# Kernel optimization log

Hardware: AMD Instinct MI355X
Metric: run time of the kernel (lower is better)

## Reference

```python
import jax, jax.numpy as jnp
from jax import lax
import numpy as np

# Architecture constants (must match init_kwargs)
K = 3            # kernel_size
F = 128          # num_filters
NL = 4           # num_layers per stage
NS = 2           # num_stages (Decoder uses TCN(num_stages=2))
DILS = [2 ** l for _ in range(NS) for l in range(NL)]  # [1,2,4,8,1,2,4,8]
NB = NS * NL     # 8 residual blocks
C_IN = 32 + 1    # dec_feat + last_y channel
D_ENC = 128
T = 32           # target_len = max_seq_len
B = 64


def _cconv(x, w, d):
    # causal dilated conv1d; x: [B, L, Cin], w: [K, Cin, Cout]
    k = w.shape[0]
    return lax.conv_general_dilated(
        x, w, window_strides=(1,), padding=[((k - 1) * d, 0)],
        rhs_dilation=(d,), dimension_numbers=('NWC', 'WIO', 'NWC'))


def setup_inputs() -> dict:
    key = jax.random.key(0)
    ks = jax.random.split(key, 20)

    def he(k, shape, fan_in):
        return jax.random.normal(k, shape, jnp.float32) * np.sqrt(2.0 / fan_in)

    inp = {
        'data_encoder': jax.random.normal(ks[0], (B, 128, D_ENC), jnp.float32),
        'data_decoder': jax.random.normal(ks[1], (B, T, C_IN - 1), jnp.float32),
        'last_y': jax.random.normal(ks[2], (B,), jnp.float32),
        # TCN block 0 (input projection block)
        'w_in': he(ks[3], (K, C_IN, F), K * C_IN),
        'b_in': jnp.zeros((F,), jnp.float32),
        'w_res': he(ks[4], (1, C_IN, F), C_IN),
        'b_res': jnp.zeros((F,), jnp.float32),
        # conv1 of blocks 1..NB-1, conv2 of all blocks
        'w1': he(ks[5], (NB - 1, K, F, F), K * F),
        'b1': jnp.zeros((NB - 1, F), jnp.float32),
        'w2': he(ks[6], (NB, K, F, F), K * F),
        'b2': jnp.zeros((NB, F), jnp.float32),
        # dense head: (F + D_ENC) -> 128 -> 64 -> 1
        'wd0': he(ks[7], (F + D_ENC, 128), F + D_ENC),
        'bd0': jnp.zeros((128,), jnp.float32),
        'wd1': he(ks[8], (128, 64), 128),
        'bd1': jnp.zeros((64,), jnp.float32),
        'wd2': he(ks[9], (64, 1), 64),
        'bd2': jnp.zeros((1,), jnp.float32),
    }
    return inp


def reference(data_encoder, data_decoder, last_y,
              w_in, b_in, w_res, b_res, w1, b1, w2, b2,
              wd0, bd0, wd1, bd1, wd2, bd2) -> jnp.ndarray:
    elu = jax.nn.elu

    def tcn(x):
        # 2 stages x 4 residual blocks of dilated causal convs; dropout off (inference)
        h = x
        for b in range(NB):
            d = DILS[b]
            if b == 0:
                c = elu(_cconv(h, w_in, d) + b_in)
                res = _cconv(h, w_res, 1) + b_res  # 1x1 channel-matching projection
            else:
                c = elu(_cconv(h, w1[b - 1], d) + b1[b - 1])
                res = h
            c = elu(_cconv(c, w2[b], d) + b2[b])
            h = elu(c + res)
        return h  # [B, L, F]

    enc_last = data_encoder[:, -1:, :]  # [B, 1, D_ENC]

    def head(t):
        L = t.shape[1]
        o = jnp.concatenate(
            [t, jnp.broadcast_to(enc_last, (t.shape[0], L, D_ENC))], axis=-1)
        o = elu(o @ wd0 + bd0)
        o = elu(o @ wd1 + bd1)
        return o @ wd2 + bd2  # [B, L, 1]

    target_len = data_decoder.shape[1]
    ly = last_y.reshape(-1, 1, 1)  # [B, 1, 1]
    cur = jnp.concatenate([data_decoder[:, :1, :], ly], axis=-1)  # [B, 1, C_IN]

    preds = []
    for i in range(target_len):  # O(T^2): reruns full TCN on growing prefix
        out = head(tcn(cur))                 # [B, i+1, 1]
        preds.append(out[:, -1, :])          # [B, 1]
        if i < target_len - 1:
            last_preds = jnp.concatenate([ly, out], axis=1)  # [B, i+2, 1]
            cur = jnp.concatenate(
                [data_decoder[:, :i + 2, :], last_preds], axis=-1)
    return jnp.concatenate(preds, axis=1)  # [B, T]
```

## Files before the change

### kernel.cpp

```cpp
#include <hip/hip_runtime.h>
#include <hip/hip_fp16.h>


constexpr int OFF_WIN  = 0;
constexpr int OFF_WRES = 24576;
constexpr int OFF_W1   = 32768;
constexpr int OFF_W2   = 376832;
constexpr int OFF_WD0  = 770048;
constexpr int OFF_WD1  = 802816;
constexpr int OFF_WD2  = 811008;
constexpr int WS_HALFS = 811072;

constexpr int O_CURX = 0;
constexpr int O_ENC  = 64;
constexpr int O_H0   = 192;
constexpr int O_H1   = 320;
constexpr int O_C1A  = 448;
constexpr int O_C1B  = 576;
constexpr int O_RES  = 704;
constexpr int O_O1   = 832;
constexpr int O_O2   = 960;
constexpr int O_IN0  = 1024;
constexpr int O_IN1  = 1152;
constexpr int O_MID0 = 8576;
constexpr int SM_FLOATS = 16256;

__device__ __forceinline__ float elu1(float x) { return x > 0.f ? x : expm1f(x); }

__device__ __forceinline__ void bar() {
    __builtin_amdgcn_sched_barrier(0);
    asm volatile("s_waitcnt lgkmcnt(0)" ::: "memory");
    __builtin_amdgcn_s_barrier();
    __builtin_amdgcn_sched_barrier(0);
}

struct W4 { float4 v[4]; };
struct W2 { float4 v[2]; };

__device__ __forceinline__ void load4(W4& w, const __half* p) {
#pragma unroll
    for (int j = 0; j < 4; ++j) w.v[j] = *(const float4*)(p + j * 1024);
}
__device__ __forceinline__ void load2(W2& w, const __half* p, int stride) {
#pragma unroll
    for (int j = 0; j < 2; ++j) w.v[j] = *(const float4*)(p + j * stride);
}

__device__ __forceinline__ float dot8(float4 wv, const float* x) {
    const __half2* h = (const __half2*)&wv;
    float2 a = __half22float2(h[0]);
    float2 b = __half22float2(h[1]);
    float2 c = __half22float2(h[2]);
    float2 d = __half22float2(h[3]);
    float4 x0 = *(const float4*)(x);
    float4 x1 = *(const float4*)(x + 4);
    return a.x * x0.x + a.y * x0.y + b.x * x0.z + b.y * x0.w +
           c.x * x1.x + c.y * x1.y + d.x * x1.z + d.y * x1.w;
}
__device__ __forceinline__ float dot4j(const W4& w, const float* x, int ks) {
    float a = dot8(w.v[0], x + ks * 8);
    a += dot8(w.v[1], x + 32 + ks * 8);
    a += dot8(w.v[2], x + 64 + ks * 8);
    a += dot8(w.v[3], x + 96 + ks * 8);
    return a;
}
__device__ __forceinline__ float dot2j(const W2& w, const float* x, int ks) {
    return dot8(w.v[0], x + ks * 8) + dot8(w.v[1], x + 32 + ks * 8);
}

__device__ __forceinline__ void loadMain(W4& w0, W4& w1, W4& w2, const __half* base_lane, int ks) {
    load4(w0, base_lane + (ks * 4) * 1024);
    load4(w1, base_lane + ((4 + ks) * 4) * 1024);
    load4(w2, base_lane + ((8 + ks) * 4) * 1024);
}

template <bool FUSE>
__device__ __forceinline__ void computeMain(const W4& w0, const W4& w1, const W4& w2,
                                            const float* x2, const float* x1, const float* x0,
                                            const float* __restrict__ bias, float* dest,
                                            const float* resv, int ch, int ks, int lane) {
    float acc = dot4j(w0, x0, ks) + dot4j(w1, x1, ks) + dot4j(w2, x2, ks);
    acc += __shfl_xor(acc, 16, 64);
    acc += __shfl_xor(acc, 32, 64);
    float v = elu1(acc + bias[ch]);
    if (FUSE) v = elu1(v + resv[ch]);
    if (lane < 16) dest[ch] = v;
}

__global__ void prep_weights(const float* __restrict__ w_in, const float* __restrict__ w_res,
                             const float* __restrict__ w1, const float* __restrict__ w2,
                             const float* __restrict__ wd0, const float* __restrict__ wd1,
                             const float* __restrict__ wd2, __half* __restrict__ dst) {
    int i = blockIdx.x * blockDim.x + threadIdx.x;
    if (i >= WS_HALFS) return;
    float v = 0.f;
    if (i < OFF_WRES) {
        int q = i, e = q & 7, ch = (q >> 3) & 127, row = (q >> 10) & 7, k = q >> 13;
        int ks = row >> 1, j = row & 1, ci = j * 32 + ks * 8 + e;
        v = (ci < 33) ? w_in[(k * 33 + ci) * 128 + ch] : 0.f;
    } else if (i < OFF_W1) {
        int q = i - OFF_WRES, e = q & 7, ch = (q >> 3) & 127, row = (q >> 10) & 7;
        int ks = row >> 1, j = row & 1, ci = j * 32 + ks * 8 + e;
        v = (ci < 33) ? w_res[ci * 128 + ch] : 0.f;
    } else if (i < OFF_W2) {
        int r = i - OFF_W1, bb = r / 49152, q = r % 49152;
        int e = q & 7, ch = (q >> 3) & 127, row = (q >> 10) & 15, k = q >> 14;
        int ks = row >> 2, j = row & 3, ci = j * 32 + ks * 8 + e;
        v = w1[((size_t)(bb * 3 + k) * 128 + ci) * 128 + ch];
    } else if (i < OFF_WD0) {
        int r = i - OFF_W2, bb = r / 49152, q = r % 49152;
        int e = q & 7, ch = (q >> 3) & 127, row = (q >> 10) & 15, k = q >> 14;
        int ks = row >> 2, j = row & 3, ci = j * 32 + ks * 8 + e;
        v = w2[((size_t)(bb * 3 + k) * 128 + ci) * 128 + ch];
    } else if (i < OFF_WD1) {
        int q = i - OFF_WD0, e = q & 7, ch = (q >> 3) & 127, row = (q >> 10) & 31;
        int ks = row >> 3, j = row & 7, ci = j * 32 + ks * 8 + e;
        v = wd0[ci * 128 + ch];
    } else if (i < OFF_WD2) {
        int q = i - OFF_WD1, e = q & 7, ch = (q >> 3) & 63, row = (q >> 9) & 15;
        int ks8 = row >> 1, j = row & 1, ci = j * 64 + ks8 * 8 + e;
        v = wd1[ci * 64 + ch];
    } else {
        v = wd2[i - OFF_WD2];
    }
    dst[i] = __float2half(v);
}

__global__ __launch_bounds__(512) void decoder_stream(
    const float* __restrict__ enc, const float* __restrict__ dec,
    const float* __restrict__ last_y, const __half* __restrict__ wsh,
    const float* __restrict__ b_in, const float* __restrict__ b_res,
    const float* __restrict__ b1, const float* __restrict__ b2,
    const float* __restrict__ bd0, const float* __restrict__ bd1,
    const float* __restrict__ bd2, float* __restrict__ out) {
    __shared__ float sm[SM_FLOATS];
    const int tid = threadIdx.x;
    const int b = blockIdx.x;
    const int lane = tid & 63;
    const int wv = tid >> 6;
    const int ch = wv * 16 + (lane & 15);
    const int ks = lane >> 4;
    const int ch64 = wv * 8 + (lane & 7);
    const int ks8 = lane >> 3;

    for (int i = tid; i < SM_FLOATS; i += 512) sm[i] = 0.f;
    __syncthreads();
    if (tid < 128) sm[O_ENC + tid] = enc[((size_t)b * 128 + 127) * 128 + tid];
    if (tid < 32) sm[O_CURX + tid] = dec[((size_t)b * 32 + 0) * 32 + tid];
    if (tid == 32) sm[O_CURX + 32] = last_y[b];
    __syncthreads();

    const float bd2v = bd2[0];
    const float wd2r = (tid < 64) ? __half2float(wsh[OFF_WD2 + tid]) : 0.f;

    W4 A0, A1, A2, B0, B1, B2;
    W2 ia0, ia1, ia2, ir, D1w;

    {
        const __half* wl = wsh + OFF_WIN + ch * 8;
        load2(ia0, wl + (ks * 2) * 1024, 1024);
        load2(ia1, wl + (8 + ks * 2) * 1024, 1024);
        load2(ia2, wl + (16 + ks * 2) * 1024, 1024);
        load2(ir, wsh + OFF_WRES + ch * 8 + (ks * 2) * 1024, 1024);
    }

#pragma unroll 1
    for (int t = 0; t < 32; ++t) {
        {
            loadMain(B0, B1, B2, wsh + OFF_W2 + ch * 8, ks);
            const float* x1 = &sm[O_IN0 + ((t - 1) & 1) * 64];
            const float* x0 = &sm[O_IN0 + (t & 1) * 64];
            float aC = dot2j(ia0, x0, ks) + dot2j(ia1, x1, ks) + dot2j(ia2, &sm[O_CURX], ks);
            float aR = dot2j(ir, &sm[O_CURX], ks);
            aC += __shfl_xor(aC, 16, 64); aC += __shfl_xor(aC, 32, 64);
            aR += __shfl_xor(aR, 16, 64); aR += __shfl_xor(aR, 32, 64);
            if (lane < 16) {
                sm[O_C1A + ch] = elu1(aC + b_in[ch]);
                sm[O_RES + ch] = aR + b_res[ch];
            }
            bar();
        }
        {
            loadMain(A0, A1, A2, wsh + OFF_W1 + ch * 8, ks);
            if (tid < 64) sm[O_IN0 + (t & 1) * 64 + tid] = sm[O_CURX + tid];
            const float* m1 = &sm[O_MID0 + ((t - 1) & 1) * 128];
            const float* m0 = &sm[O_MID0 + (t & 1) * 128];
            computeMain<true>(B0, B1, B2, &sm[O_C1A], m1, m0, b2, &sm[O_H1], &sm[O_RES],
                              ch, ks, lane);
            bar();
        }
        int inB = O_IN1, midBprev = O_MID0, midB = O_MID0 + 256, mprev = 2;
#pragma unroll 1
        for (int blk = 1; blk < 8; ++blk) {
            const int d = 1 << (blk & 3);
            const int m = 2 * d;
            const int p = blk & 1;
            float* Hp = &sm[p ? O_H1 : O_H0];
            float* Hq = &sm[p ? O_H0 : O_H1];
            float* C1p = &sm[p ? O_C1B : O_C1A];
            float* C1q = &sm[p ? O_C1A : O_C1B];
            loadMain(B0, B1, B2, wsh + OFF_W2 + blk * 49152 + ch * 8, ks);
            if (tid < 128) sm[midBprev + (t & (mprev - 1)) * 128 + tid] = C1q[tid];
            {
                const float* x1 = &sm[inB + ((t - d) & (m - 1)) * 128];
                const float* x0 = &sm[inB + (t & (m - 1)) * 128];
                computeMain<false>(A0, A1, A2, Hp, x1, x0, b1 + (blk - 1) * 128, C1p, Hp,
                                   ch, ks, lane);
            }
            bar();
            if (blk < 7) {
                loadMain(A0, A1, A2, wsh + OFF_W1 + blk * 49152 + ch * 8, ks);
            } else {
                const __half* pd0 = wsh + OFF_WD0 + ch * 8;
                load4(A0, pd0 + (ks * 8) * 1024);
                load4(A1, pd0 + (ks * 8 + 4) * 1024);
            }
            if (tid < 128) sm[inB + (t & (m - 1)) * 128 + tid] = Hp[tid];
            {
                const float* m1 = &sm[midB + ((t - d) & (m - 1)) * 128];
                const float* m0 = &sm[midB + (t & (m - 1)) * 128];
                computeMain<true>(B0, B1, B2, C1p, m1, m0, b2 + blk * 128, Hq, Hp,
                                  ch, ks, lane);
            }
            bar();
            inB += m * 128; midBprev = midB; midB += m * 128; mprev = m;
        }
        {
            const __half* pd1 = wsh + OFF_WD1 + ch64 * 8 + (ks8 * 2) * 512;
            load2(D1w, pd1, 512);
            if (tid < 128) sm[midBprev + (t & (mprev - 1)) * 128 + tid] = sm[O_C1B + tid];
            float acc = dot4j(A0, &sm[O_H0], ks) + dot4j(A1, &sm[O_ENC], ks);
            acc += __shfl_xor(acc, 16, 64);
            acc += __shfl_xor(acc, 32, 64);
            if (lane < 16) sm[O_O1 + ch] = elu1(acc + bd0[ch]);
            bar();
        }
        {
            const __half* wl = wsh + OFF_WIN + ch * 8;
            load2(ia0, wl + (ks * 2) * 1024, 1024);
            load2(ia1, wl + (8 + ks * 2) * 1024, 1024);
            load2(ia2, wl + (16 + ks * 2) * 1024, 1024);
            load2(ir, wsh + OFF_WRES + ch * 8 + (ks * 2) * 1024, 1024);
            float acc = dot8(D1w.v[0], &sm[O_O1 + ks8 * 8]) +
                        dot8(D1w.v[1], &sm[O_O1 + 64 + ks8 * 8]);
            acc += __shfl_xor(acc, 8, 64);
            acc += __shfl_xor(acc, 16, 64);
            acc += __shfl_xor(acc, 32, 64);
            if (lane < 8) sm[O_O2 + ch64] = elu1(acc + bd1[ch64]);
            int tn = t < 31 ? t + 1 : 31;
            if (tid < 32) sm[O_CURX + tid] = dec[((size_t)b * 32 + tn) * 32 + tid];
            bar();
        }
        if (tid < 64) {
            float v = sm[O_O2 + tid] * wd2r;
#pragma unroll
            for (int off = 32; off; off >>= 1) v += __shfl_xor(v, off, 64);
            if (tid == 0) {
                float pr = v + bd2v;
                out[b * 32 + t] = pr;
                sm[O_CURX + 32] = pr;
            }
        }
        bar();
    }
}

extern "C" void kernel_launch(void* const* d_in, const int* in_sizes, int n_in,
                              void* d_out, int out_size, void* d_ws, size_t ws_size,
                              hipStream_t stream) {
    const float* enc    = (const float*)d_in[0];
    const float* dec    = (const float*)d_in[1];
    const float* last_y = (const float*)d_in[2];
    const float* w_in   = (const float*)d_in[3];
    const float* b_in   = (const float*)d_in[4];
    const float* w_res  = (const float*)d_in[5];
    const float* b_res  = (const float*)d_in[6];
    const float* w1     = (const float*)d_in[7];
    const float* b1     = (const float*)d_in[8];
    const float* w2     = (const float*)d_in[9];
    const float* b2     = (const float*)d_in[10];
    const float* wd0    = (const float*)d_in[11];
    const float* bd0    = (const float*)d_in[12];
    const float* wd1    = (const float*)d_in[13];
    const float* bd1    = (const float*)d_in[14];
    const float* wd2    = (const float*)d_in[15];
    const float* bd2    = (const float*)d_in[16];
    float* out = (float*)d_out;
    __half* wsh = (__half*)d_ws;

    prep_weights<<<(WS_HALFS + 255) / 256, 256, 0, stream>>>(w_in, w_res, w1, w2, wd0, wd1,
                                                             wd2, wsh);
    decoder_stream<<<64, 512, 0, stream>>>(enc, dec, last_y, wsh, b_in, b_res, b1, b2, bd0,
                                           bd1, bd2, out);
}
```

Measured before the change: 1.462 ms.

## Use MFMA 16x16x32 f16 for the per-step TCN convolutions

Replaces the scalar fp16-to-fp32 dot-product matvecs with MFMA f16 instructions. Each wave computes 16 output channels, with activations stored in shared memory as fp16 and weights repacked into the MFMA B-fragment layout. Biases move into registers, the block loop is fully unrolled, and the residual state stays in registers. Only row 0 of each MFMA tile is useful because the batch per block is one sample, so most MFMA work is wasted. Activations are now kept in fp16 rather than fp32, which lowers their precision.

```diff
diff --git a/kernel.cpp b/kernel.cpp
--- a/kernel.cpp
+++ b/kernel.cpp
@@ -1,6 +1,11 @@
 #include <hip/hip_runtime.h>
 #include <hip/hip_fp16.h>
 
+
+typedef _Float16 f16;
+typedef __attribute__((ext_vector_type(8))) _Float16 f16x8;
+typedef __attribute__((ext_vector_type(4))) float f32x4;
+#define MFMA16(a, b, c) __builtin_amdgcn_mfma_f32_16x16x32_f16((a), (b), (c), 0, 0, 0)
 
 constexpr int OFF_WIN  = 0;
 constexpr int OFF_WRES = 24576;
@@ -11,19 +16,18 @@
 constexpr int OFF_WD2  = 811008;
 constexpr int WS_HALFS = 811072;
 
-constexpr int O_CURX = 0;
-constexpr int O_ENC  = 64;
-constexpr int O_H0   = 192;
-constexpr int O_H1   = 320;
-constexpr int O_C1A  = 448;
-constexpr int O_C1B  = 576;
-constexpr int O_RES  = 704;
-constexpr int O_O1   = 832;
-constexpr int O_O2   = 960;
-constexpr int O_IN0  = 1024;
-constexpr int O_IN1  = 1152;
-constexpr int O_MID0 = 8576;
-constexpr int SM_FLOATS = 16256;
+constexpr int H_CURX = 0;
+constexpr int H_ENC  = 64;
+constexpr int H_H0   = 192;
+constexpr int H_H1   = 320;
+constexpr int H_C1A  = 448;
+constexpr int H_C1B  = 576;
+constexpr int H_O1   = 704;
+constexpr int H_IN0  = 832;
+constexpr int INO[8]  = {0, 960, 1472, 2496, 4544, 4800, 5312, 6336};
+constexpr int MIDO[8] = {8384, 8640, 9152, 10176, 12224, 12480, 12992, 14016};
+constexpr int SMH_HALFS = 16064;
+constexpr int DIL[8] = {1, 2, 4, 8, 1, 2, 4, 8};
 
 __device__ __forceinline__ float elu1(float x) { return x > 0.f ? x : expm1f(x); }
 
@@ -34,231 +38,220 @@
     __builtin_amdgcn_sched_barrier(0);
 }
 
-struct W4 { float4 v[4]; };
-struct W2 { float4 v[2]; };
-
-__device__ __forceinline__ void load4(W4& w, const __half* p) {
-#pragma unroll
-    for (int j = 0; j < 4; ++j) w.v[j] = *(const float4*)(p + j * 1024);
-}
-__device__ __forceinline__ void load2(W2& w, const __half* p, int stride) {
-#pragma unroll
-    for (int j = 0; j < 2; ++j) w.v[j] = *(const float4*)(p + j * stride);
-}
-
-__device__ __forceinline__ float dot8(float4 wv, const float* x) {
-    const __half2* h = (const __half2*)&wv;
-    float2 a = __half22float2(h[0]);
-    float2 b = __half22float2(h[1]);
-    float2 c = __half22float2(h[2]);
-    float2 d = __half22float2(h[3]);
-    float4 x0 = *(const float4*)(x);
-    float4 x1 = *(const float4*)(x + 4);
-    return a.x * x0.x + a.y * x0.y + b.x * x0.z + b.y * x0.w +
-           c.x * x1.x + c.y * x1.y + d.x * x1.z + d.y * x1.w;
-}
-__device__ __forceinline__ float dot4j(const W4& w, const float* x, int ks) {
-    float a = dot8(w.v[0], x + ks * 8);
-    a += dot8(w.v[1], x + 32 + ks * 8);
-    a += dot8(w.v[2], x + 64 + ks * 8);
-    a += dot8(w.v[3], x + 96 + ks * 8);
-    return a;
-}
-__device__ __forceinline__ float dot2j(const W2& w, const float* x, int ks) {
-    return dot8(w.v[0], x + ks * 8) + dot8(w.v[1], x + 32 + ks * 8);
-}
-
-__device__ __forceinline__ void loadMain(W4& w0, W4& w1, W4& w2, const __half* base_lane, int ks) {
-    load4(w0, base_lane + (ks * 4) * 1024);
-    load4(w1, base_lane + ((4 + ks) * 4) * 1024);
-    load4(w2, base_lane + ((8 + ks) * 4) * 1024);
-}
-
-template <bool FUSE>
-__device__ __forceinline__ void computeMain(const W4& w0, const W4& w1, const W4& w2,
-                                            const float* x2, const float* x1, const float* x0,
-                                            const float* __restrict__ bias, float* dest,
-                                            const float* resv, int ch, int ks, int lane) {
-    float acc = dot4j(w0, x0, ks) + dot4j(w1, x1, ks) + dot4j(w2, x2, ks);
-    acc += __shfl_xor(acc, 16, 64);
-    acc += __shfl_xor(acc, 32, 64);
-    float v = elu1(acc + bias[ch]);
-    if (FUSE) v = elu1(v + resv[ch]);
-    if (lane < 16) dest[ch] = v;
+struct W12 { f16x8 v[12]; };
+
+template <int N>
+__device__ __forceinline__ void loadWn(W12& w, const f16* __restrict__ p) {
+#pragma unroll
+    for (int j = 0; j < N; ++j) w.v[j] = *(const f16x8*)(p + j * 512);
+}
+__device__ __forceinline__ void loadS0(W12& w, const f16* __restrict__ wsh, int nt, int lane) {
+    const f16* p1 = wsh + OFF_WIN + nt * 3072 + lane * 8;
+#pragma unroll
+    for (int j = 0; j < 6; ++j) w.v[j] = *(const f16x8*)(p1 + j * 512);
+    const f16* p2 = wsh + OFF_WRES + nt * 1024 + lane * 8;
+#pragma unroll
+    for (int j = 0; j < 2; ++j) w.v[6 + j] = *(const f16x8*)(p2 + j * 512);
+}
+
+__device__ __forceinline__ void conv12(f32x4& acc, const W12& w, const f16* smh,
+                                       int b2d, int b1d, int b0, int g8) {
+#pragma unroll
+    for (int kk = 0; kk < 12; ++kk) {
+        int base = (kk < 4) ? b2d : (kk < 8 ? b1d : b0);
+        f16x8 a = *(const f16x8*)(smh + base + (kk & 3) * 32 + g8);
+        acc = MFMA16(a, w.v[kk], acc);
+    }
 }
 
 __global__ void prep_weights(const float* __restrict__ w_in, const float* __restrict__ w_res,
                              const float* __restrict__ w1, const float* __restrict__ w2,
                              const float* __restrict__ wd0, const float* __restrict__ wd1,
-                             const float* __restrict__ wd2, __half* __restrict__ dst) {
+                             const float* __restrict__ wd2, f16* __restrict__ dst) {
     int i = blockIdx.x * blockDim.x + threadIdx.x;
     if (i >= WS_HALFS) return;
     float v = 0.f;
     if (i < OFF_WRES) {
-        int q = i, e = q & 7, ch = (q >> 3) & 127, row = (q >> 10) & 7, k = q >> 13;
-        int ks = row >> 1, j = row & 1, ci = j * 32 + ks * 8 + e;
-        v = (ci < 33) ? w_in[(k * 33 + ci) * 128 + ch] : 0.f;
+        int e = i & 7, l = (i >> 3) & 63, r = i >> 9;
+        int kk = r % 6, nt = r / 6;
+        int tap = kk >> 1, ci = (kk & 1) * 32 + ((l >> 4) << 3) + e, ch = nt * 16 + (l & 15);
+        v = (ci < 33) ? w_in[(tap * 33 + ci) * 128 + ch] : 0.f;
     } else if (i < OFF_W1) {
-        int q = i - OFF_WRES, e = q & 7, ch = (q >> 3) & 127, row = (q >> 10) & 7;
-        int ks = row >> 1, j = row & 1, ci = j * 32 + ks * 8 + e;
+        int q = i - OFF_WRES, e = q & 7, l = (q >> 3) & 63, r = q >> 9;
+        int kk = r & 1, nt = r >> 1;
+        int ci = kk * 32 + ((l >> 4) << 3) + e, ch = nt * 16 + (l & 15);
         v = (ci < 33) ? w_res[ci * 128 + ch] : 0.f;
     } else if (i < OFF_W2) {
-        int r = i - OFF_W1, bb = r / 49152, q = r % 49152;
-        int e = q & 7, ch = (q >> 3) & 127, row = (q >> 10) & 15, k = q >> 14;
-        int ks = row >> 2, j = row & 3, ci = j * 32 + ks * 8 + e;
-        v = w1[((size_t)(bb * 3 + k) * 128 + ci) * 128 + ch];
+        int q = i - OFF_W1, bb = q / 49152, s = q % 49152;
+        int e = s & 7, l = (s >> 3) & 63, r = s >> 9;
+        int kk = r % 12, nt = r / 12;
+        int tap = kk >> 2, ci = (kk & 3) * 32 + ((l >> 4) << 3) + e, ch = nt * 16 + (l & 15);
+        v = w1[((size_t)(bb * 3 + tap) * 128 + ci) * 128 + ch];
     } else if (i < OFF_WD0) {
-        int r = i - OFF_W2, bb = r / 49152, q = r % 49152;
-        int e = q & 7, ch = (q >> 3) & 127, row = (q >> 10) & 15, k = q >> 14;
-        int ks = row >> 2, j = row & 3, ci = j * 32 + ks * 8 + e;
-        v = w2[((size_t)(bb * 3 + k) * 128 + ci) * 128 + ch];
+        int q = i - OFF_W2, bb = q / 49152, s = q % 49152;
+        int e = s & 7, l = (s >> 3) & 63, r = s >> 9;
+        int kk = r % 12, nt = r / 12;
+        int tap = kk >> 2, ci = (kk & 3) * 32 + ((l >> 4) << 3) + e, ch = nt * 16 + (l & 15);
+        v = w2[((size_t)(bb * 3 + tap) * 128 + ci) * 128 + ch];
     } else if (i < OFF_WD1) {
-        int q = i - OFF_WD0, e = q & 7, ch = (q >> 3) & 127, row = (q >> 10) & 31;
-        int ks = row >> 3, j = row & 7, ci = j * 32 + ks * 8 + e;
-        v = wd0[ci * 128 + ch];
+        int q = i - OFF_WD0, e = q & 7, l = (q >> 3) & 63, r = q >> 9;
+        int kk = r & 7, nt = r >> 3;
+        int ci = kk * 32 + ((l >> 4) << 3) + e;
+        v = wd0[ci * 128 + nt * 16 + (l & 15)];
     } else if (i < OFF_WD2) {
-        int q = i - OFF_WD1, e = q & 7, ch = (q >> 3) & 63, row = (q >> 9) & 15;
-        int ks8 = row >> 1, j = row & 1, ci = j * 64 + ks8 * 8 + e;
+        int q = i - OFF_WD1, e = q & 7, l = (q >> 3) & 63, r = q >> 9;
+        int kk = r & 3, nt = r >> 2;
+        int ci = kk * 32 + ((l >> 4) << 3) + e, ch = nt * 16 + (l & 15);
         v = wd1[ci * 64 + ch];
     } else {
         v = wd2[i - OFF_WD2];
     }
-    dst[i] = __float2half(v);
+    dst[i] = (f16)v;
 }
 
 __global__ __launch_bounds__(512) void decoder_stream(
     const float* __restrict__ enc, const float* __restrict__ dec,
-    const float* __restrict__ last_y, const __half* __restrict__ wsh,
+    const float* __restrict__ last_y, const f16* __restrict__ wsh,
     const float* __restrict__ b_in, const float* __restrict__ b_res,
     const float* __restrict__ b1, const float* __restrict__ b2,
     const float* __restrict__ bd0, const float* __restrict__ bd1,
-    const float* __restrict__ bd2, float* __restrict__ out) {
-    __shared__ float sm[SM_FLOATS];
+    const float* __restrict__ bd2, const float* __restrict__ wd2,
+    float* __restrict__ out) {
+    __shared__ f16 smh[SMH_HALFS];
+    __shared__ float smf[64];
     const int tid = threadIdx.x;
     const int b = blockIdx.x;
     const int lane = tid & 63;
-    const int wv = tid >> 6;
-    const int ch = wv * 16 + (lane & 15);
-    const int ks = lane >> 4;
-    const int ch64 = wv * 8 + (lane & 7);
-    const int ks8 = lane >> 3;
-
-    for (int i = tid; i < SM_FLOATS; i += 512) sm[i] = 0.f;
+    const int nt = tid >> 6;
+    const int g8 = ((lane >> 4) << 3);
+    const int ch = nt * 16 + (lane & 15);
+
+    for (int i = tid; i < SMH_HALFS / 2; i += 512) ((unsigned int*)smh)[i] = 0u;
     __syncthreads();
-    if (tid < 128) sm[O_ENC + tid] = enc[((size_t)b * 128 + 127) * 128 + tid];
-    if (tid < 32) sm[O_CURX + tid] = dec[((size_t)b * 32 + 0) * 32 + tid];
-    if (tid == 32) sm[O_CURX + 32] = last_y[b];
+    if (tid < 128) smh[H_ENC + tid] = (f16)enc[((size_t)b * 128 + 127) * 128 + tid];
+    if (tid < 32) smh[H_CURX + tid] = (f16)dec[(size_t)b * 32 * 32 + tid];
+    if (tid == 32) smh[H_CURX + 32] = (f16)last_y[b];
     __syncthreads();
 
+    const float rb_in = b_in[ch], rb_res = b_res[ch], rbd0 = bd0[ch];
+    const float rbd1 = bd1[ch & 63];
+    float rb1[7], rb2[8];
+#pragma unroll
+    for (int j = 0; j < 7; ++j) rb1[j] = b1[j * 128 + ch];
+#pragma unroll
+    for (int j = 0; j < 8; ++j) rb2[j] = b2[j * 128 + ch];
+    const float wd2r = (tid < 64) ? wd2[tid] : 0.f;
     const float bd2v = bd2[0];
-    const float wd2r = (tid < 64) ? __half2float(wsh[OFF_WD2 + tid]) : 0.f;
-
-    W4 A0, A1, A2, B0, B1, B2;
-    W2 ia0, ia1, ia2, ir, D1w;
-
-    {
-        const __half* wl = wsh + OFF_WIN + ch * 8;
-        load2(ia0, wl + (ks * 2) * 1024, 1024);
-        load2(ia1, wl + (8 + ks * 2) * 1024, 1024);
-        load2(ia2, wl + (16 + ks * 2) * 1024, 1024);
-        load2(ir, wsh + OFF_WRES + ch * 8 + (ks * 2) * 1024, 1024);
-    }
+
+    W12 P, Q;
+    loadS0(P, wsh, nt, lane);
+    float hreg = 0.f, resreg = 0.f;
 
 #pragma unroll 1
     for (int t = 0; t < 32; ++t) {
         {
-            loadMain(B0, B1, B2, wsh + OFF_W2 + ch * 8, ks);
-            const float* x1 = &sm[O_IN0 + ((t - 1) & 1) * 64];
-            const float* x0 = &sm[O_IN0 + (t & 1) * 64];
-            float aC = dot2j(ia0, x0, ks) + dot2j(ia1, x1, ks) + dot2j(ia2, &sm[O_CURX], ks);
-            float aR = dot2j(ir, &sm[O_CURX], ks);
-            aC += __shfl_xor(aC, 16, 64); aC += __shfl_xor(aC, 32, 64);
-            aR += __shfl_xor(aR, 16, 64); aR += __shfl_xor(aR, 32, 64);
-            if (lane < 16) {
-                sm[O_C1A + ch] = elu1(aC + b_in[ch]);
-                sm[O_RES + ch] = aR + b_res[ch];
-            }
-            bar();
-        }
-        {
-            loadMain(A0, A1, A2, wsh + OFF_W1 + ch * 8, ks);
-            if (tid < 64) sm[O_IN0 + (t & 1) * 64 + tid] = sm[O_CURX + tid];
-            const float* m1 = &sm[O_MID0 + ((t - 1) & 1) * 128];
-            const float* m0 = &sm[O_MID0 + (t & 1) * 128];
-            computeMain<true>(B0, B1, B2, &sm[O_C1A], m1, m0, b2, &sm[O_H1], &sm[O_RES],
-                              ch, ks, lane);
-            bar();
-        }
-        int inB = O_IN1, midBprev = O_MID0, midB = O_MID0 + 256, mprev = 2;
-#pragma unroll 1
+            loadWn<12>(Q, wsh + OFF_W2 + nt * 6144 + lane * 8);
+            const int a2d = H_IN0 + (t & 1) * 64;
+            const int a1d = H_IN0 + ((t - 1) & 1) * 64;
+            f32x4 aC = {0.f, 0.f, 0.f, 0.f}, aR = {0.f, 0.f, 0.f, 0.f};
+#pragma unroll
+            for (int kk = 0; kk < 6; ++kk) {
+                int base = (kk < 2) ? a2d : (kk < 4 ? a1d : H_CURX);
+                f16x8 a = *(const f16x8*)(smh + base + (kk & 1) * 32 + g8);
+                aC = MFMA16(a, P.v[kk], aC);
+            }
+#pragma unroll
+            for (int kk = 0; kk < 2; ++kk) {
+                f16x8 a = *(const f16x8*)(smh + H_CURX + kk * 32 + g8);
+                aR = MFMA16(a, P.v[6 + kk], aR);
+            }
+            float c1 = elu1(aC[0] + rb_in);
+            resreg = aR[0] + rb_res;
+            if (lane < 16) smh[H_C1A + ch] = (f16)c1;
+            bar();
+        }
+        {
+            loadWn<12>(P, wsh + OFF_W1 + nt * 6144 + lane * 8);
+            if (tid < 64) smh[H_IN0 + (t & 1) * 64 + tid] = smh[H_CURX + tid];
+            f32x4 acc = {0.f, 0.f, 0.f, 0.f};
+            conv12(acc, Q, smh, MIDO[0] + (t & 1) * 128, MIDO[0] + ((t - 1) & 1) * 128,
+                   H_C1A, g8);
+            float v = elu1(acc[0] + rb2[0]);
+            hreg = elu1(v + resreg);
+            if (lane < 16) smh[H_H1 + ch] = (f16)hreg;
+            bar();
+        }
+#pragma unroll
         for (int blk = 1; blk < 8; ++blk) {
-            const int d = 1 << (blk & 3);
-            const int m = 2 * d;
+            const int d = DIL[blk], m = 2 * d;
+            const int mprev = 2 * DIL[blk - 1];
             const int p = blk & 1;
-            float* Hp = &sm[p ? O_H1 : O_H0];
-            float* Hq = &sm[p ? O_H0 : O_H1];
-            float* C1p = &sm[p ? O_C1B : O_C1A];
-            float* C1q = &sm[p ? O_C1A : O_C1B];
-            loadMain(B0, B1, B2, wsh + OFF_W2 + blk * 49152 + ch * 8, ks);
-            if (tid < 128) sm[midBprev + (t & (mprev - 1)) * 128 + tid] = C1q[tid];
+            const int Hp = p ? H_H1 : H_H0, Hq = p ? H_H0 : H_H1;
+            const int C1p = p ? H_C1B : H_C1A, C1q = p ? H_C1A : H_C1B;
             {
-                const float* x1 = &sm[inB + ((t - d) & (m - 1)) * 128];
-                const float* x0 = &sm[inB + (t & (m - 1)) * 128];
-                computeMain<false>(A0, A1, A2, Hp, x1, x0, b1 + (blk - 1) * 128, C1p, Hp,
-                                   ch, ks, lane);
-            }
-            bar();
-            if (blk < 7) {
-                loadMain(A0, A1, A2, wsh + OFF_W1 + blk * 49152 + ch * 8, ks);
-            } else {
-                const __half* pd0 = wsh + OFF_WD0 + ch * 8;
-                load4(A0, pd0 + (ks * 8) * 1024);
-                load4(A1, pd0 + (ks * 8 + 4) * 1024);
-            }
-            if (tid < 128) sm[inB + (t & (m - 1)) * 128 + tid] = Hp[tid];
+                loadWn<12>(Q, wsh + OFF_W2 + blk * 49152 + nt * 6144 + lane * 8);
+                if (tid < 128)
+                    smh[MIDO[blk - 1] + (t & (mprev - 1)) * 128 + tid] = smh[C1q + tid];
+                f32x4 acc = {0.f, 0.f, 0.f, 0.f};
+                conv12(acc, P, smh, INO[blk] + (t & (m - 1)) * 128,
+                       INO[blk] + ((t - d) & (m - 1)) * 128, Hp, g8);
+                float c1 = elu1(acc[0] + rb1[blk - 1]);
+                if (lane < 16) smh[C1p + ch] = (f16)c1;
+                bar();
+            }
             {
-                const float* m1 = &sm[midB + ((t - d) & (m - 1)) * 128];
-                const float* m0 = &sm[midB + (t & (m - 1)) * 128];
-                computeMain<true>(B0, B1, B2, C1p, m1, m0, b2 + blk * 128, Hq, Hp,
-                                  ch, ks, lane);
-            }
-            bar();
-            inB += m * 128; midBprev = midB; midB += m * 128; mprev = m;
-        }
-        {
-            const __half* pd1 = wsh + OFF_WD1 + ch64 * 8 + (ks8 * 2) * 512;
-            load2(D1w, pd1, 512);
-            if (tid < 128) sm[midBprev + (t & (mprev - 1)) * 128 + tid] = sm[O_C1B + tid];
-            float acc = dot4j(A0, &sm[O_H0], ks) + dot4j(A1, &sm[O_ENC], ks);
-            acc += __shfl_xor(acc, 16, 64);
-            acc += __shfl_xor(acc, 32, 64);
-            if (lane < 16) sm[O_O1 + ch] = elu1(acc + bd0[ch]);
-            bar();
-        }
-        {
-            const __half* wl = wsh + OFF_WIN + ch * 8;
-            load2(ia0, wl + (ks * 2) * 1024, 1024);
-            load2(ia1, wl + (8 + ks * 2) * 1024, 1024);
-            load2(ia2, wl + (16 + ks * 2) * 1024, 1024);
-            load2(ir, wsh + OFF_WRES + ch * 8 + (ks * 2) * 1024, 1024);
-            float acc = dot8(D1w.v[0], &sm[O_O1 + ks8 * 8]) +
-                        dot8(D1w.v[1], &sm[O_O1 + 64 + ks8 * 8]);
-            acc += __shfl_xor(acc, 8, 64);
-            acc += __shfl_xor(acc, 16, 64);
-            acc += __shfl_xor(acc, 32, 64);
-            if (lane < 8) sm[O_O2 + ch64] = elu1(acc + bd1[ch64]);
+                if (blk < 7) loadWn<12>(P, wsh + OFF_W1 + blk * 49152 + nt * 6144 + lane * 8);
+                else loadWn<8>(P, wsh + OFF_WD0 + nt * 4096 + lane * 8);
+                if (tid < 128)
+                    smh[INO[blk] + (t & (m - 1)) * 128 + tid] = smh[Hp + tid];
+                f32x4 acc = {0.f, 0.f, 0.f, 0.f};
+                conv12(acc, Q, smh, MIDO[blk] + (t & (m - 1)) * 128,
+                       MIDO[blk] + ((t - d) & (m - 1)) * 128, C1p, g8);
+                float v = elu1(acc[0] + rb2[blk]);
+                hreg = elu1(v + hreg);
+                if (lane < 16) smh[Hq + ch] = (f16)hreg;
+                bar();
+            }
+        }
+        {
+            loadWn<4>(Q, wsh + OFF_WD1 + (nt & 3) * 2048 + lane * 8);
+            if (tid < 128)
+                smh[MIDO[7] + (t & 15) * 128 + tid] = smh[H_C1B + tid];
+            f32x4 acc = {0.f, 0.f, 0.f, 0.f};
+#pragma unroll
+            for (int kk = 0; kk < 8; ++kk) {
+                int base = (kk < 4) ? (H_H0 + kk * 32) : (H_ENC + (kk - 4) * 32);
+                f16x8 a = *(const f16x8*)(smh + base + g8);
+                acc = MFMA16(a, P.v[kk], acc);
+            }
+            float v = elu1(acc[0] + rbd0);
+            if (lane < 16) smh[H_O1 + ch] = (f16)v;
+            bar();
+        }
+        {
+            loadS0(P, wsh, nt, lane);
+            if (nt < 4) {
+                f32x4 acc = {0.f, 0.f, 0.f, 0.f};
+#pragma unroll
+                for (int kk = 0; kk < 4; ++kk) {
+                    f16x8 a = *(const f16x8*)(smh + H_O1 + kk * 32 + g8);
+                    acc = MFMA16(a, Q.v[kk], acc);
+                }
+                float v = elu1(acc[0] + rbd1);
+                if (lane < 16) smf[ch] = v;
+            }
             int tn = t < 31 ? t + 1 : 31;
-            if (tid < 32) sm[O_CURX + tid] = dec[((size_t)b * 32 + tn) * 32 + tid];
+            if (tid < 32) smh[H_CURX + tid] = (f16)dec[((size_t)b * 32 + tn) * 32 + tid];
             bar();
         }
         if (tid < 64) {
-            float v = sm[O_O2 + tid] * wd2r;
+            float v = smf[tid] * wd2r;
 #pragma unroll
             for (int off = 32; off; off >>= 1) v += __shfl_xor(v, off, 64);
             if (tid == 0) {
                 float pr = v + bd2v;
                 out[b * 32 + t] = pr;
-                sm[O_CURX + 32] = pr;
+                smh[H_CURX + 32] = (f16)pr;
             }
         }
         bar();
@@ -286,10 +279,10 @@
     const float* wd2    = (const float*)d_in[15];
     const float* bd2    = (const float*)d_in[16];
     float* out = (float*)d_out;
-    __half* wsh = (__half*)d_ws;
+    f16* wsh = (f16*)d_ws;
 
     prep_weights<<<(WS_HALFS + 255) / 256, 256, 0, stream>>>(w_in, w_res, w1, w2, wd0, wd1,
                                                              wd2, wsh);
     decoder_stream<<<64, 512, 0, stream>>>(enc, dec, last_y, wsh, b_in, b_res, b1, b2, bd0,
-                                           bd1, bd2, out);
-}
+                                           bd1, bd2, wd2, out);
+}
```

Measured after the change: 1.990 ms. +36.1%, slower.
